# Kernel optimization log

Hardware: AMD Instinct MI355X
Metric: run time of the kernel (lower is better)

## Reference

```python
import jax, jax.numpy as jnp
import numpy as np

THRESHOLD = 6.2
N_SECTIONS = 9      # n_conv_sections
SEC_LEN = 4         # n_section_length
SEC_H = 9           # n_input_sections + n_section_length - 1
BATCH = 16384


def setup_inputs() -> dict:
    key = jax.random.key(0)
    k1, k2 = jax.random.split(key)
    # input spike-wave tensor [T, C=1, H=41, W=40]
    x = jax.random.uniform(k1, (BATCH, 1, 41, 40), dtype=jnp.float32)
    # per-section conv weights, N(0.8, 0.05) as in snn.Convolution init
    W = 0.8 + 0.05 * jax.random.normal(k2, (N_SECTIONS, 50, 1, 6, 40), dtype=jnp.float32)
    return {"x": x, "W": W}


def _conv(sec, w):
    # sec: [B,1,9,40], w: [50,1,6,40] -> [B,50,4,1]
    return jax.lax.conv_general_dilated(
        sec, w, window_strides=(1, 1), padding='VALID',
        dimension_numbers=('NCHW', 'OIHW', 'NCHW'))


def reference(x, W):
    # slice the 9 overlapping input sections -> [9, B, 1, 9, 40]
    sec = jnp.stack([x[:, :, i * SEC_LEN:i * SEC_LEN + SEC_H, :]
                     for i in range(N_SECTIONS)])
    pots = jax.vmap(_conv)(sec, W)                      # [9, B, 50, 4, 1]
    pots = jnp.max(pots, axis=3, keepdims=True)         # Pooling((4,1)) -> [9, B, 50, 1, 1]
    spks = jnp.where(pots > THRESHOLD, 1.0, 0.0).astype(pots.dtype)
    # concat sections along height (dim=2 of [B,C,H,W])
    pots_cat = jnp.moveaxis(pots[:, :, :, 0, :], 0, 2)  # [B, 50, 9, 1]
    spks_cat = jnp.moveaxis(spks[:, :, :, 0, :], 0, 2)  # [B, 50, 9, 1]
    return pots_cat, spks_cat
```

## Files before the change

kernel.cpp:

```cpp
#include <hip/hip_runtime.h>
#include <cstdint>
#include <cstddef>

#define NBATCH   16384
#define NSEC     9
#define NOC      50
#define NOCP     64
#define KPAD     256
#define KREAL    240
#define XROW     1640
#define XUNITS   208
#define XSF      1664
#define TB       16
#define OUTHALF  7372800
#define THRESH   6.2f

typedef _Float16 half8  __attribute__((ext_vector_type(8)));
typedef float    f32x4  __attribute__((ext_vector_type(4)));

__global__ __launch_bounds__(256)
void wconv_kernel(const float* __restrict__ W, _Float16* __restrict__ wks) {
    int idx = blockIdx.x * 256 + threadIdx.x;
    int k   = idx & 255;
    int ocp = (idx >> 8) & 63;
    int sec = idx >> 14;
    float v = 0.0f;
    if (ocp < NOC && k < KREAL)
        v = W[(size_t)(sec * NOC + ocp) * KREAL + k];
    wks[idx] = (_Float16)v;
}

__global__ __launch_bounds__(256, 3)
void fused_kernel(const float* __restrict__ x,
                  const _Float16* __restrict__ wks,
                  float* __restrict__ out) {
    __shared__ __align__(16) _Float16 xs[TB * XSF];

    const int tid = threadIdx.x;
    const size_t b0 = (size_t)blockIdx.x * TB;

    {
        const int bb  = tid >> 4;
        const int u16 = tid & 15;
        const int sw  = bb & 7;
        const float* xrow = x + (b0 + bb) * XROW;
        _Float16* lrow = xs + bb * XSF;

        #pragma unroll
        for (int c = 0; c < 2; ++c) {
            const int jn = c ? 6 : 7;
            float4 va[7], vb[7];
            #pragma unroll
            for (int jj = 0; jj < 7; ++jj) {
                if (jj < jn) {
                    int u = u16 + 16 * (c * 7 + jj);
                    if (u < 205) {
                        va[jj] = *(const float4*)(xrow + u * 8);
                        vb[jj] = *(const float4*)(xrow + u * 8 + 4);
                    } else {
                        va[jj] = float4{0, 0, 0, 0};
                        vb[jj] = float4{0, 0, 0, 0};
                    }
                }
            }
            #pragma unroll
            for (int jj = 0; jj < 7; ++jj) {
                if (jj < jn) {
                    int u = u16 + 16 * (c * 7 + jj);
                    half8 h;
                    h[0] = (_Float16)va[jj].x; h[1] = (_Float16)va[jj].y;
                    h[2] = (_Float16)va[jj].z; h[3] = (_Float16)va[jj].w;
                    h[4] = (_Float16)vb[jj].x; h[5] = (_Float16)vb[jj].y;
                    h[6] = (_Float16)vb[jj].z; h[7] = (_Float16)vb[jj].w;
                    *(half8*)(lrow + ((u ^ sw) << 3)) = h;
                }
            }
        }
    }
    __syncthreads();

    const int lane = tid & 63;
    const int w    = tid >> 6;
    const int l15  = lane & 15;
    const int quad = lane >> 4;
    const int sw   = l15 & 7;

    const _Float16* arow = xs + l15 * XSF;
    const _Float16* wrow = wks + (size_t)(w * 16 + l15) * KPAD + quad * 8;

    f32x4 res[NSEC];

    for (int s = 0; s < NSEC; ++s) {
        const _Float16* wsec = wrow + (size_t)s * (NOCP * KPAD);
        half8 bv[8];
        #pragma unroll
        for (int kk = 0; kk < 8; ++kk)
            bv[kk] = *(const half8*)(wsec + kk * 32);

        f32x4 acc[4] = {f32x4{}, f32x4{}, f32x4{}, f32x4{}};
        const int su = s * 20 + quad;
        #pragma unroll
        for (int kk = 0; kk < 8; ++kk) {
            #pragma unroll
            for (int h = 0; h < 4; ++h) {
                int unit = su + h * 5 + kk * 4;
                half8 av = *(const half8*)(arow + ((unit ^ sw) << 3));
                acc[h] = __builtin_amdgcn_mfma_f32_16x16x32_f16(
                             av, bv[kk], acc[h], 0, 0, 0);
            }
        }
        f32x4 r;
        #pragma unroll
        for (int j = 0; j < 4; ++j)
            r[j] = fmaxf(fmaxf(acc[0][j], acc[1][j]),
                         fmaxf(acc[2][j], acc[3][j]));
        res[s] = r;
    }

    __syncthreads();
    float* t = (float*)xs;
    const int oc = w * 16 + l15;
    if (oc < NOC) {
        #pragma unroll
        for (int s = 0; s < NSEC; ++s)
            #pragma unroll
            for (int r = 0; r < 4; ++r)
                t[(quad * 4 + r) * 450 + oc * 9 + s] = res[s][r];
    }
    __syncthreads();

    const size_t ob = b0 * 450;
    for (int i = tid; i < TB * 450; i += 256) {
        float v = t[i];
        out[ob + i] = v;
        out[OUTHALF + ob + i] = (v > THRESH) ? 1.0f : 0.0f;
    }
}

__global__ __launch_bounds__(256)
void naive_kernel(const float* __restrict__ x, const float* __restrict__ W,
                  float* __restrict__ out) {
    size_t idx = (size_t)blockIdx.x * 256 + threadIdx.x;
    if (idx >= OUTHALF) return;
    int s  = (int)(idx % NSEC);
    int oc = (int)((idx / NSEC) % NOC);
    int b  = (int)(idx / (NSEC * NOC));
    const float* xb = x + (size_t)b * XROW + s * 160;
    const float* wv = W + (size_t)(s * NOC + oc) * KREAL;
    float best = -1e30f;
    for (int h0 = 0; h0 < 4; ++h0) {
        float acc = 0.0f;
        for (int k = 0; k < KREAL; ++k)
            acc += xb[h0 * 40 + k] * wv[k];
        best = fmaxf(best, acc);
    }
    out[idx] = best;
    out[OUTHALF + idx] = (best > THRESH) ? 1.0f : 0.0f;
}

extern "C" void kernel_launch(void* const* d_in, const int* in_sizes, int n_in,
                              void* d_out, int out_size, void* d_ws, size_t ws_size,
                              hipStream_t stream) {
    const float* x = (const float*)d_in[0];
    const float* W = (const float*)d_in[1];
    float* out = (float*)d_out;

    const size_t w_bytes = (size_t)NSEC * NOCP * KPAD * sizeof(_Float16);

    if (ws_size < w_bytes) {
        naive_kernel<<<(OUTHALF + 255) / 256, 256, 0, stream>>>(x, W, out);
        return;
    }

    _Float16* wks = (_Float16*)d_ws;

    wconv_kernel<<<(NSEC * NOCP * KPAD) / 256, 256, 0, stream>>>(W, wks);
    fused_kernel<<<NBATCH / TB, 256, 0, stream>>>(x, wks, out);
}
```

Before: 213.4 us.

## Restructure MFMA tiling with 2x2 register blocking and pipelined loads

Measured after the change: 233.3 us. +9.3%, slower.

```diff
diff --git a/kernel.cpp b/kernel.cpp
--- a/kernel.cpp
+++ b/kernel.cpp
@@ -18,6 +18,15 @@
 typedef _Float16 half8  __attribute__((ext_vector_type(8)));
 typedef float    f32x4  __attribute__((ext_vector_type(4)));
 
+__device__ inline half8 cvt8(float4 a, float4 b) {
+    half8 h;
+    h[0] = (_Float16)a.x; h[1] = (_Float16)a.y;
+    h[2] = (_Float16)a.z; h[3] = (_Float16)a.w;
+    h[4] = (_Float16)b.x; h[5] = (_Float16)b.y;
+    h[6] = (_Float16)b.z; h[7] = (_Float16)b.w;
+    return h;
+}
+
 __global__ __launch_bounds__(256)
 void wconv_kernel(const float* __restrict__ W, _Float16* __restrict__ wks) {
     int idx = blockIdx.x * 256 + threadIdx.x;
@@ -39,101 +48,162 @@
     const int tid = threadIdx.x;
     const size_t b0 = (size_t)blockIdx.x * TB;
 
-    {
-        const int bb  = tid >> 4;
-        const int u16 = tid & 15;
-        const int sw  = bb & 7;
-        const float* xrow = x + (b0 + bb) * XROW;
-        _Float16* lrow = xs + bb * XSF;
-
+    const int bb  = tid >> 4;
+    const int u16 = tid & 15;
+    const int ssw = bb & 7;
+    const float* xrow = x + (b0 + bb) * XROW;
+    _Float16* lrow = xs + bb * XSF;
+
+    const int lane  = tid & 63;
+    const int w     = tid >> 6;
+    const int l15   = lane & 15;
+    const int quad  = lane >> 4;
+    const int mbase = 8 * (w >> 1);
+    const int nbase = 32 * (w & 1);
+
+    const int row0 = mbase + (l15 >> 2);
+    const int row1 = row0 + 4;
+    const _Float16* arow0 = xs + row0 * XSF;
+    const _Float16* arow1 = xs + row1 * XSF;
+    const int sw0 = row0 & 7;
+    const int sw1 = row1 & 7;
+    const int ubase = (l15 & 3) * 5 + quad;
+
+    const _Float16* wb = wks + (size_t)(nbase + l15) * KPAD + quad * 8;
+
+    float4 va[7], vb[7];
+    #pragma unroll
+    for (int j = 0; j < 7; ++j) {
+        int u = u16 + 16 * j;
+        va[j] = *(const float4*)(xrow + u * 8);
+        vb[j] = *(const float4*)(xrow + u * 8 + 4);
+    }
+
+    half8 bv[2][2][4];
+    #pragma unroll
+    for (int nt = 0; nt < 2; ++nt)
         #pragma unroll
-        for (int c = 0; c < 2; ++c) {
-            const int jn = c ? 6 : 7;
-            float4 va[7], vb[7];
-            #pragma unroll
-            for (int jj = 0; jj < 7; ++jj) {
-                if (jj < jn) {
-                    int u = u16 + 16 * (c * 7 + jj);
-                    if (u < 205) {
-                        va[jj] = *(const float4*)(xrow + u * 8);
-                        vb[jj] = *(const float4*)(xrow + u * 8 + 4);
-                    } else {
-                        va[jj] = float4{0, 0, 0, 0};
-                        vb[jj] = float4{0, 0, 0, 0};
-                    }
-                }
-            }
-            #pragma unroll
-            for (int jj = 0; jj < 7; ++jj) {
-                if (jj < jn) {
-                    int u = u16 + 16 * (c * 7 + jj);
-                    half8 h;
-                    h[0] = (_Float16)va[jj].x; h[1] = (_Float16)va[jj].y;
-                    h[2] = (_Float16)va[jj].z; h[3] = (_Float16)va[jj].w;
-                    h[4] = (_Float16)vb[jj].x; h[5] = (_Float16)vb[jj].y;
-                    h[6] = (_Float16)vb[jj].z; h[7] = (_Float16)vb[jj].w;
-                    *(half8*)(lrow + ((u ^ sw) << 3)) = h;
-                }
-            }
-        }
+        for (int kk = 0; kk < 4; ++kk)
+            bv[0][nt][kk] = *(const half8*)(wb + (size_t)(nt * 16) * KPAD + kk * 32);
+
+    #pragma unroll
+    for (int j = 0; j < 7; ++j) {
+        int u = u16 + 16 * j;
+        *(half8*)(lrow + ((u ^ ssw) << 3)) = cvt8(va[j], vb[j]);
     }
     __syncthreads();
 
-    const int lane = tid & 63;
-    const int w    = tid >> 6;
-    const int l15  = lane & 15;
-    const int quad = lane >> 4;
-    const int sw   = l15 & 7;
-
-    const _Float16* arow = xs + l15 * XSF;
-    const _Float16* wrow = wks + (size_t)(w * 16 + l15) * KPAD + quad * 8;
-
-    f32x4 res[NSEC];
-
-    for (int s = 0; s < NSEC; ++s) {
-        const _Float16* wsec = wrow + (size_t)s * (NOCP * KPAD);
-        half8 bv[8];
+    float res[NSEC][2][2];
+    f32x4 acc[2][2];
+    float4 wa[6], wc[6];
+
+    #pragma unroll
+    for (int c = 0; c < 18; ++c) {
+        const int s = c >> 1, half = c & 1;
+
+        if (c < 17) {
+            const int ns = (c + 1) >> 1, nh = (c + 1) & 1;
+            const _Float16* wsec = wb + (size_t)(ns * NOCP) * KPAD + nh * 128;
+            #pragma unroll
+            for (int nt = 0; nt < 2; ++nt)
+                #pragma unroll
+                for (int kk = 0; kk < 4; ++kk)
+                    bv[(c + 1) & 1][nt][kk] =
+                        *(const half8*)(wsec + (size_t)(nt * 16) * KPAD + kk * 32);
+        }
+        if (c == 1) {
+            #pragma unroll
+            for (int j = 0; j < 3; ++j) {
+                int u = u16 + 16 * (j + 7);
+                if (u < 205) {
+                    wa[j] = *(const float4*)(xrow + u * 8);
+                    wc[j] = *(const float4*)(xrow + u * 8 + 4);
+                } else { wa[j] = float4{0,0,0,0}; wc[j] = float4{0,0,0,0}; }
+            }
+        }
+        if (c == 4) {
+            #pragma unroll
+            for (int j = 0; j < 3; ++j) {
+                int u = u16 + 16 * (j + 7);
+                *(half8*)(lrow + ((u ^ ssw) << 3)) = cvt8(wa[j], wc[j]);
+            }
+            #pragma unroll
+            for (int j = 3; j < 6; ++j) {
+                int u = u16 + 16 * (j + 7);
+                if (u < 205) {
+                    wa[j] = *(const float4*)(xrow + u * 8);
+                    wc[j] = *(const float4*)(xrow + u * 8 + 4);
+                } else { wa[j] = float4{0,0,0,0}; wc[j] = float4{0,0,0,0}; }
+            }
+        }
+
+        if (half == 0) {
+            acc[0][0] = f32x4{}; acc[0][1] = f32x4{};
+            acc[1][0] = f32x4{}; acc[1][1] = f32x4{};
+        }
         #pragma unroll
-        for (int kk = 0; kk < 8; ++kk)
-            bv[kk] = *(const half8*)(wsec + kk * 32);
-
-        f32x4 acc[4] = {f32x4{}, f32x4{}, f32x4{}, f32x4{}};
-        const int su = s * 20 + quad;
+        for (int kk = 0; kk < 4; ++kk) {
+            const int unit = s * 20 + (half * 4 + kk) * 4 + ubase;
+            half8 av0 = *(const half8*)(arow0 + ((unit ^ sw0) << 3));
+            half8 av1 = *(const half8*)(arow1 + ((unit ^ sw1) << 3));
+            acc[0][0] = __builtin_amdgcn_mfma_f32_16x16x32_f16(
+                            av0, bv[c & 1][0][kk], acc[0][0], 0, 0, 0);
+            acc[0][1] = __builtin_amdgcn_mfma_f32_16x16x32_f16(
+                            av0, bv[c & 1][1][kk], acc[0][1], 0, 0, 0);
+            acc[1][0] = __builtin_amdgcn_mfma_f32_16x16x32_f16(
+                            av1, bv[c & 1][0][kk], acc[1][0], 0, 0, 0);
+            acc[1][1] = __builtin_amdgcn_mfma_f32_16x16x32_f16(
+                            av1, bv[c & 1][1][kk], acc[1][1], 0, 0, 0);
+        }
+        if (half == 1) {
+            #pragma unroll
+            for (int mt = 0; mt < 2; ++mt)
+                #pragma unroll
+                for (int nt = 0; nt < 2; ++nt)
+                    res[s][mt][nt] =
+                        fmaxf(fmaxf(acc[mt][nt][0], acc[mt][nt][1]),
+                              fmaxf(acc[mt][nt][2], acc[mt][nt][3]));
+        }
+        if (c == 7) {
+            #pragma unroll
+            for (int j = 3; j < 6; ++j) {
+                int u = u16 + 16 * (j + 7);
+                *(half8*)(lrow + ((u ^ ssw) << 3)) = cvt8(wa[j], wc[j]);
+            }
+            __syncthreads();
+        }
+    }
+
+    __syncthreads();
+    float* tb = (float*)xs;
+    #pragma unroll
+    for (int mt = 0; mt < 2; ++mt) {
+        const int bl = mbase + 4 * mt + quad;
         #pragma unroll
-        for (int kk = 0; kk < 8; ++kk) {
-            #pragma unroll
-            for (int h = 0; h < 4; ++h) {
-                int unit = su + h * 5 + kk * 4;
-                half8 av = *(const half8*)(arow + ((unit ^ sw) << 3));
-                acc[h] = __builtin_amdgcn_mfma_f32_16x16x32_f16(
-                             av, bv[kk], acc[h], 0, 0, 0);
-            }
-        }
-        f32x4 r;
-        #pragma unroll
-        for (int j = 0; j < 4; ++j)
-            r[j] = fmaxf(fmaxf(acc[0][j], acc[1][j]),
-                         fmaxf(acc[2][j], acc[3][j]));
-        res[s] = r;
-    }
-
+        for (int nt = 0; nt < 2; ++nt) {
+            const int oc = nbase + nt * 16 + l15;
+            if (oc < NOC) {
+                #pragma unroll
+                for (int s = 0; s < NSEC; ++s)
+                    tb[bl * 450 + oc * 9 + s] = res[s][mt][nt];
+            }
+        }
+    }
     __syncthreads();
-    float* t = (float*)xs;
-    const int oc = w * 16 + l15;
-    if (oc < NOC) {
-        #pragma unroll
-        for (int s = 0; s < NSEC; ++s)
-            #pragma unroll
-            for (int r = 0; r < 4; ++r)
-                t[(quad * 4 + r) * 450 + oc * 9 + s] = res[s][r];
-    }
-    __syncthreads();
 
     const size_t ob = b0 * 450;
-    for (int i = tid; i < TB * 450; i += 256) {
-        float v = t[i];
-        out[ob + i] = v;
-        out[OUTHALF + ob + i] = (v > THRESH) ? 1.0f : 0.0f;
+    const float4* t4 = (const float4*)tb;
+    float4* o4  = (float4*)(out + ob);
+    float4* o4s = (float4*)(out + OUTHALF + ob);
+    for (int i = tid; i < TB * 450 / 4; i += 256) {
+        float4 v = t4[i];
+        o4[i] = v;
+        float4 sp;
+        sp.x = (v.x > THRESH) ? 1.0f : 0.0f;
+        sp.y = (v.y > THRESH) ? 1.0f : 0.0f;
+        sp.z = (v.z > THRESH) ? 1.0f : 0.0f;
+        sp.w = (v.w > THRESH) ? 1.0f : 0.0f;
+        o4s[i] = sp;
     }
 }
 
```
